# Optimization experiments

Hardware: AMD Instinct MI355X
Metric: run time of the kernel (lower is better)

The kernel has to match this reference:

```python
import jax, jax.numpy as jnp
import numpy as np

B, T, I, H, O, P = 32, 8192, 16, 128, 3, 1024


def setup_inputs() -> dict:
    key = jax.random.key(0)
    ks = jax.random.split(key, 8)
    x = jax.random.normal(ks[0], (B, T, I), dtype=jnp.float32)
    # feature channel 2 holds the photo id (original code does x[:,:,2].long())
    ids = jax.random.randint(ks[1], (B, T), 0, P)
    x = x.at[:, :, 2].set(ids.astype(jnp.float32))
    s = 1.0 / np.sqrt(H).astype(np.float32)
    W_ih = jax.random.uniform(ks[2], (4 * H, I), minval=-s, maxval=s, dtype=jnp.float32)
    W_hh = jax.random.uniform(ks[3], (4 * H, H), minval=-s, maxval=s, dtype=jnp.float32)
    b_ih = jax.random.uniform(ks[4], (4 * H,), minval=-s, maxval=s, dtype=jnp.float32)
    b_hh = jax.random.uniform(ks[5], (4 * H,), minval=-s, maxval=s, dtype=jnp.float32)
    W_fc = jax.random.uniform(ks[6], (O, H), minval=-s, maxval=s, dtype=jnp.float32)
    b_fc = jax.random.uniform(ks[7], (O,), minval=-s, maxval=s, dtype=jnp.float32)
    return dict(x=x, W_ih=W_ih, W_hh=W_hh, b_ih=b_ih, b_hh=b_hh,
                W_fc=W_fc, b_fc=b_fc, num_photos=P)


def _lstm(x, W_ih, W_hh, b_ih, b_hh):
    # single-layer batch_first LSTM, PyTorch gate order (i, f, g, o), zero init state
    Bz = x.shape[0]
    Hh = W_hh.shape[1]
    # precompute input contribution for all timesteps: [B, T, 4H]
    xg = jnp.einsum('bti,gi->btg', x, W_ih) + b_ih + b_hh

    def step(carry, gx):
        h, c = carry
        g = gx + h @ W_hh.T
        i, f, gg, o = jnp.split(g, 4, axis=-1)
        i = jax.nn.sigmoid(i)
        f = jax.nn.sigmoid(f)
        gg = jnp.tanh(gg)
        o = jax.nn.sigmoid(o)
        c = f * c + i * gg
        h = o * jnp.tanh(c)
        return (h, c), h

    h0 = jnp.zeros((Bz, Hh), x.dtype)
    _, hs = jax.lax.scan(step, (h0, h0), jnp.swapaxes(xg, 0, 1))  # [T, B, H]
    return jnp.swapaxes(hs, 0, 1)  # [B, T, H]


def reference(x, W_ih, W_hh, b_ih, b_hh, W_fc, b_fc, num_photos):
    Bz, T, _ = x.shape
    h = _lstm(x, W_ih, W_hh, b_ih, b_hh)          # [B, T, H]
    out = h @ W_fc.T + b_fc                        # [B, T, 3]
    ids = x[:, :, 2].astype(jnp.int32)             # [B, T]
    valid = ids < num_photos
    safe = jnp.where(valid, ids, 0)
    # flatten (batch, photo_id) into a single segment id per element
    seg = (jnp.arange(Bz, dtype=jnp.int32)[:, None] * num_photos + safe).reshape(-1)
    w = valid.astype(out.dtype)
    sums = jax.ops.segment_sum((out * w[..., None]).reshape(-1, out.shape[-1]),
                               seg, num_segments=Bz * num_photos)
    sums = sums.reshape(Bz, num_photos, out.shape[-1])
    counts = jax.ops.segment_sum(w.reshape(-1), seg, num_segments=Bz * num_photos)
    counts = counts.reshape(Bz, num_photos, 1)
    counts = jnp.where(counts == 0, 1.0, counts)   # matches photo_counts[photo_counts==0]=1
    return sums / counts
```

## Files before the change

### kernel.cpp

```cpp
#include <hip/hip_runtime.h>

#define B_ 32
#define T_ 8192
#define I_ 16
#define H_ 128
#define P_ 1024
#define O_ 3

typedef _Float16 h2 __attribute__((ext_vector_type(2)));
typedef _Float16 h4 __attribute__((ext_vector_type(4)));
typedef _Float16 h8 __attribute__((ext_vector_type(8)));

#if __has_builtin(__builtin_amdgcn_fdot2)
#define FDOT2(a, b, c) __builtin_amdgcn_fdot2((a), (b), (c), false)
#else
__device__ __forceinline__ float fdot2_asm(h2 a, h2 b, float c) {
    asm("v_dot2_f32_f16 %0, %1, %2, %0" : "+v"(c) : "v"(a), "v"(b));
    return c;
}
#define FDOT2(a, b, c) fdot2_asm((a), (b), (c))
#endif

#define FORME(M, g) M(g,0,0) M(g,0,1) M(g,0,2) M(g,0,3) \
                    M(g,1,0) M(g,1,1) M(g,1,2) M(g,1,3) \
                    M(g,2,0) M(g,2,1) M(g,2,2) M(g,2,3) \
                    M(g,3,0) M(g,3,1) M(g,3,2) M(g,3,3)
#define FORALL(M) FORME(M,0) FORME(M,1) FORME(M,2) FORME(M,3)
#define FORG(M) M(0) M(1) M(2) M(3)

#define DPPF(v, ctrl) \
    __int_as_float(__builtin_amdgcn_mov_dpp(__float_as_int(v), (ctrl), 0xF, 0xF, true))
#define SWZF(v, imm) \
    __int_as_float(__builtin_amdgcn_ds_swizzle(__float_as_int(v), (imm)))

__device__ __forceinline__ float tanh_f(float x) {
    return 2.f / (1.f + __expf(-2.f * x)) - 1.f;
}
__device__ __forceinline__ h4 cvt4(float4 v) {
    return (h4){(_Float16)v.x, (_Float16)v.y, (_Float16)v.z, (_Float16)v.w};
}

__device__ __forceinline__ void lds_barrier() {
    asm volatile("s_waitcnt lgkmcnt(0)\n\ts_barrier" ::: "memory");
}

__global__ __launch_bounds__(512, 2) __attribute__((amdgpu_waves_per_eu(2, 2)))
void lstm_fused(
    const float* __restrict__ x,
    const float* __restrict__ W_ih,
    const float* __restrict__ W_hh,
    const float* __restrict__ b_ih,
    const float* __restrict__ b_hh,
    const float* __restrict__ W_fc,
    float* __restrict__ sums,
    float* __restrict__ counts)
{
    const int b   = blockIdx.x;
    const int tid = threadIdx.x;
    const int j   = tid >> 2;
    const int kc  = tid & 3;

    __shared__ __align__(16) _Float16 hh[2][H_];
    __shared__ __align__(16) _Float16 xt[2][16 * I_];
    __shared__ float sums_lds[P_ * O_];
    __shared__ float counts_lds[P_];

    const float* wr0 = W_hh + (0 * H_ + j) * H_;
    const float* wr1 = W_hh + (1 * H_ + j) * H_;
    const float* wr2 = W_hh + (2 * H_ + j) * H_;
    const float* wr3 = W_hh + (3 * H_ + j) * H_;
    #define WLOAD(g, m, e) h2 W##g##_##m##_##e = (h2){ \
        (_Float16)wr##g[kc * 8 + 32 * (m) + 2 * (e)], \
        (_Float16)wr##g[kc * 8 + 32 * (m) + 2 * (e) + 1]};
    FORALL(WLOAD)

    #define ULOAD(g) \
        h2 U##g##_0 = (h2){(_Float16)W_ih[((g) * H_ + j) * I_ + kc * 4 + 0], \
                           (_Float16)W_ih[((g) * H_ + j) * I_ + kc * 4 + 1]}; \
        h2 U##g##_1 = (h2){(_Float16)W_ih[((g) * H_ + j) * I_ + kc * 4 + 2], \
                           (_Float16)W_ih[((g) * H_ + j) * I_ + kc * 4 + 3]};
    FORG(ULOAD)

    const float bias = b_ih[kc * H_ + j] + b_hh[kc * H_ + j];
    const float wfc  = (kc < 3) ? W_fc[kc * H_ + j] : 0.f;

    for (int i = tid; i < P_ * O_; i += 512) sums_lds[i] = 0.f;
    for (int i = tid; i < P_;      i += 512) counts_lds[i] = 0.f;
    if (tid < H_) hh[0][tid] = (_Float16)0.f;

    const float* xb = x + (size_t)b * T_ * I_;
    float4 xr4 = make_float4(0.f, 0.f, 0.f, 0.f);
    if (tid < 64) {
        xr4 = ((const float4*)xb)[tid];
        *(h4*)&xt[0][tid * 4] = cvt4(xr4);
    }
    float c = 0.f;
    __syncthreads();

    #pragma unroll 1
    for (int t = 0; t < T_; ++t) {
        const int off = t & 15;
        const int btx = (t >> 4) & 1;
        const int bh  = t & 1;

        if (tid < 64) {
            if (off == 0 && t + 16 < T_)
                xr4 = ((const float4*)(xb + (t + 16) * I_))[tid];
            if (off == 8 && t + 8 < T_)
                *(h4*)&xt[btx ^ 1][tid * 4] = cvt4(xr4);
        }

        const h4 xv4 = *(const h4*)&xt[btx][off * I_ + kc * 4];
        const h2 xv0 = __builtin_shufflevector(xv4, xv4, 0, 1);
        const h2 xv1 = __builtin_shufflevector(xv4, xv4, 2, 3);
        const int id = (int)(float)xt[btx][off * I_ + 2];

        float acc0 = 0.f, acc1 = 0.f, acc2 = 0.f, acc3 = 0.f;
        #define HD(m) { \
            h8 hv = *(const h8*)&hh[bh][kc * 8 + 32 * (m)]; \
            h2 p0 = __builtin_shufflevector(hv, hv, 0, 1); \
            h2 p1 = __builtin_shufflevector(hv, hv, 2, 3); \
            h2 p2 = __builtin_shufflevector(hv, hv, 4, 5); \
            h2 p3 = __builtin_shufflevector(hv, hv, 6, 7); \
            acc0 = FDOT2(p0, W0_##m##_0, acc0); acc0 = FDOT2(p1, W0_##m##_1, acc0); \
            acc0 = FDOT2(p2, W0_##m##_2, acc0); acc0 = FDOT2(p3, W0_##m##_3, acc0); \
            acc1 = FDOT2(p0, W1_##m##_0, acc1); acc1 = FDOT2(p1, W1_##m##_1, acc1); \
            acc1 = FDOT2(p2, W1_##m##_2, acc1); acc1 = FDOT2(p3, W1_##m##_3, acc1); \
            acc2 = FDOT2(p0, W2_##m##_0, acc2); acc2 = FDOT2(p1, W2_##m##_1, acc2); \
            acc2 = FDOT2(p2, W2_##m##_2, acc2); acc2 = FDOT2(p3, W2_##m##_3, acc2); \
            acc3 = FDOT2(p0, W3_##m##_0, acc3); acc3 = FDOT2(p1, W3_##m##_1, acc3); \
            acc3 = FDOT2(p2, W3_##m##_2, acc3); acc3 = FDOT2(p3, W3_##m##_3, acc3); }
        HD(0) HD(1) HD(2) HD(3)
        acc0 = FDOT2(xv0, U0_0, acc0); acc0 = FDOT2(xv1, U0_1, acc0);
        acc1 = FDOT2(xv0, U1_0, acc1); acc1 = FDOT2(xv1, U1_1, acc1);
        acc2 = FDOT2(xv0, U2_0, acc2); acc2 = FDOT2(xv1, U2_1, acc2);
        acc3 = FDOT2(xv0, U3_0, acc3); acc3 = FDOT2(xv1, U3_1, acc3);

        float s_;
        s_ = DPPF(acc0, 0xB1); acc0 += s_;
        s_ = DPPF(acc1, 0xB1); acc1 += s_;
        s_ = DPPF(acc2, 0xB1); acc2 += s_;
        s_ = DPPF(acc3, 0xB1); acc3 += s_;
        s_ = DPPF(acc0, 0x4E); acc0 += s_;
        s_ = DPPF(acc1, 0x4E); acc1 += s_;
        s_ = DPPF(acc2, 0x4E); acc2 += s_;
        s_ = DPPF(acc3, 0x4E); acc3 += s_;

        float tg = (kc == 0) ? acc0 : (kc == 1) ? acc1 : (kc == 2) ? acc2 : acc3;
        tg += bias;
        const bool  isg = (kc == 2);
        const float arg = isg ? (tg + tg) : tg;
        const float sf  = 1.f / (1.f + __expf(-arg));
        const float act = isg ? (sf + sf - 1.f) : sf;

        const float gi = DPPF(act, 0x00);
        const float gf = DPPF(act, 0x55);
        const float gg = DPPF(act, 0xAA);
        const float go = DPPF(act, 0xFF);
        c = fmaf(gf, c, gi * gg);
        const float hnew = go * tanh_f(c);

        if (kc == 0) hh[bh ^ 1][j] = (_Float16)hnew;

        float p = hnew * wfc;
        p += SWZF(p, 0x101F);
        p += SWZF(p, 0x201F);
        p += SWZF(p, 0x401F);
        p += __shfl_xor(p, 32, 64);
        const bool idv = ((unsigned)id < P_);
        if (((tid & 63) < 3) && idv)
            atomicAdd(&sums_lds[id * O_ + (tid & 63)], p);
        if (tid == 0 && idv)
            atomicAdd(&counts_lds[id], 1.f);

        lds_barrier();
    }

    float* sums_g = sums + (size_t)b * P_ * O_;
    for (int i = tid; i < P_ * O_; i += 512) sums_g[i] = sums_lds[i];
    float* cnt_g = counts + (size_t)b * P_;
    for (int i = tid; i < P_; i += 512) cnt_g[i] = counts_lds[i];
}

__global__ void finalize_kernel(const float* __restrict__ sums,
                                const float* __restrict__ counts,
                                const float* __restrict__ b_fc,
                                float* __restrict__ out)
{
    const int idx = blockIdx.x * blockDim.x + threadIdx.x;
    if (idx >= B_ * P_ * O_) return;
    const int o  = idx % O_;
    const int bp = idx / O_;
    const float cnt = counts[bp];
    const float denom = (cnt > 0.f) ? cnt : 1.f;
    out[idx] = (sums[idx] + cnt * b_fc[o]) / denom;
}

extern "C" void kernel_launch(void* const* d_in, const int* in_sizes, int n_in,
                              void* d_out, int out_size, void* d_ws, size_t ws_size,
                              hipStream_t stream) {
    const float* x    = (const float*)d_in[0];
    const float* W_ih = (const float*)d_in[1];
    const float* W_hh = (const float*)d_in[2];
    const float* b_ih = (const float*)d_in[3];
    const float* b_hh = (const float*)d_in[4];
    const float* W_fc = (const float*)d_in[5];
    const float* b_fc = (const float*)d_in[6];

    float* out    = (float*)d_out;
    float* sums   = (float*)d_ws;
    float* counts = sums + (size_t)B_ * P_ * O_;

    lstm_fused<<<B_, 512, 0, stream>>>(x, W_ih, W_hh, b_ih, b_hh, W_fc, sums, counts);

    const int n = B_ * P_ * O_;
    finalize_kernel<<<(n + 255) / 256, 256, 0, stream>>>(sums, counts, b_fc, out);
}
```

Before: 6.346 ms.

## Batch four sequences per block and compute LSTM recurrence with MFMA

Replaces the per-sequence fdot2 recurrence with 16x16x32 f16 MFMA instructions, processing four batch sequences per block (8 blocks instead of 32), with N columns replicated across the four sequences. Gate preactivations, bias, and the input projection are folded into MFMA accumulation, and the hidden state is stored in a skewed LDS layout to avoid bank conflicts. Segment atomics are deferred one step to overlap with the next step's compute. This trades parallelism across CUs for matrix-core throughput, so the serial per-step latency now decides the speed.

```diff
diff --git a/kernel.cpp b/kernel.cpp
--- a/kernel.cpp
+++ b/kernel.cpp
@@ -6,45 +6,35 @@
 #define H_ 128
 #define P_ 1024
 #define O_ 3
-
-typedef _Float16 h2 __attribute__((ext_vector_type(2)));
-typedef _Float16 h4 __attribute__((ext_vector_type(4)));
-typedef _Float16 h8 __attribute__((ext_vector_type(8)));
-
-#if __has_builtin(__builtin_amdgcn_fdot2)
-#define FDOT2(a, b, c) __builtin_amdgcn_fdot2((a), (b), (c), false)
-#else
-__device__ __forceinline__ float fdot2_asm(h2 a, h2 b, float c) {
-    asm("v_dot2_f32_f16 %0, %1, %2, %0" : "+v"(c) : "v"(a), "v"(b));
-    return c;
-}
-#define FDOT2(a, b, c) fdot2_asm((a), (b), (c))
-#endif
-
-#define FORME(M, g) M(g,0,0) M(g,0,1) M(g,0,2) M(g,0,3) \
-                    M(g,1,0) M(g,1,1) M(g,1,2) M(g,1,3) \
-                    M(g,2,0) M(g,2,1) M(g,2,2) M(g,2,3) \
-                    M(g,3,0) M(g,3,1) M(g,3,2) M(g,3,3)
-#define FORALL(M) FORME(M,0) FORME(M,1) FORME(M,2) FORME(M,3)
-#define FORG(M) M(0) M(1) M(2) M(3)
-
-#define DPPF(v, ctrl) \
-    __int_as_float(__builtin_amdgcn_mov_dpp(__float_as_int(v), (ctrl), 0xF, 0xF, true))
+#define NB 4
+#define BLOCKS (B_ / NB)
+
+typedef _Float16 h4v __attribute__((ext_vector_type(4)));
+typedef _Float16 h8v __attribute__((ext_vector_type(8)));
+typedef float f4v __attribute__((ext_vector_type(4)));
+
 #define SWZF(v, imm) \
     __int_as_float(__builtin_amdgcn_ds_swizzle(__float_as_int(v), (imm)))
-
+__device__ __forceinline__ float xor32_add(float p) {
+    float a = p, b = p;
+    asm("v_permlane32_swap_b32 %0, %1" : "+v"(a), "+v"(b));
+    return a + b;
+}
+
+__device__ __forceinline__ float sigf(float x) {
+    return 1.f / (1.f + __expf(-x));
+}
 __device__ __forceinline__ float tanh_f(float x) {
     return 2.f / (1.f + __expf(-2.f * x)) - 1.f;
 }
-__device__ __forceinline__ h4 cvt4(float4 v) {
-    return (h4){(_Float16)v.x, (_Float16)v.y, (_Float16)v.z, (_Float16)v.w};
-}
-
+__device__ __forceinline__ h4v cvt4(float4 v) {
+    return (h4v){(_Float16)v.x, (_Float16)v.y, (_Float16)v.z, (_Float16)v.w};
+}
 __device__ __forceinline__ void lds_barrier() {
     asm volatile("s_waitcnt lgkmcnt(0)\n\ts_barrier" ::: "memory");
 }
 
-__global__ __launch_bounds__(512, 2) __attribute__((amdgpu_waves_per_eu(2, 2)))
+__global__ __launch_bounds__(512, 2)
 void lstm_fused(
     const float* __restrict__ x,
     const float* __restrict__ W_ih,
@@ -55,131 +45,175 @@
     float* __restrict__ sums,
     float* __restrict__ counts)
 {
-    const int b   = blockIdx.x;
-    const int tid = threadIdx.x;
-    const int j   = tid >> 2;
-    const int kc  = tid & 3;
-
-    __shared__ __align__(16) _Float16 hh[2][H_];
-    __shared__ __align__(16) _Float16 xt[2][16 * I_];
-    __shared__ float sums_lds[P_ * O_];
-    __shared__ float counts_lds[P_];
-
-    const float* wr0 = W_hh + (0 * H_ + j) * H_;
-    const float* wr1 = W_hh + (1 * H_ + j) * H_;
-    const float* wr2 = W_hh + (2 * H_ + j) * H_;
-    const float* wr3 = W_hh + (3 * H_ + j) * H_;
-    #define WLOAD(g, m, e) h2 W##g##_##m##_##e = (h2){ \
-        (_Float16)wr##g[kc * 8 + 32 * (m) + 2 * (e)], \
-        (_Float16)wr##g[kc * 8 + 32 * (m) + 2 * (e) + 1]};
-    FORALL(WLOAD)
-
-    #define ULOAD(g) \
-        h2 U##g##_0 = (h2){(_Float16)W_ih[((g) * H_ + j) * I_ + kc * 4 + 0], \
-                           (_Float16)W_ih[((g) * H_ + j) * I_ + kc * 4 + 1]}; \
-        h2 U##g##_1 = (h2){(_Float16)W_ih[((g) * H_ + j) * I_ + kc * 4 + 2], \
-                           (_Float16)W_ih[((g) * H_ + j) * I_ + kc * 4 + 3]};
-    FORG(ULOAD)
-
-    const float bias = b_ih[kc * H_ + j] + b_hh[kc * H_ + j];
-    const float wfc  = (kc < 3) ? W_fc[kc * H_ + j] : 0.f;
-
-    for (int i = tid; i < P_ * O_; i += 512) sums_lds[i] = 0.f;
-    for (int i = tid; i < P_;      i += 512) counts_lds[i] = 0.f;
-    if (tid < H_) hh[0][tid] = (_Float16)0.f;
-
-    const float* xb = x + (size_t)b * T_ * I_;
+    const int bx   = blockIdx.x;
+    const int tid  = threadIdx.x;
+    const int w    = tid >> 6;
+    const int lane = tid & 63;
+    const int n    = lane & 15;
+    const int gh   = lane >> 4;
+    const int j0   = 16 * w + 4 * gh;
+
+    __shared__ float sums_lds[NB][P_ * O_];
+    __shared__ float counts_lds[NB][P_];
+    __shared__ __align__(16) _Float16 Hlds[2][16][H_];
+    __shared__ __align__(16) _Float16 xt[2][16][NB][I_];
+
+    h8v A[4][5];
+    #pragma unroll
+    for (int G = 0; G < 4; ++G) {
+        const int row = 128 * G + 16 * w + n;
+        const float* wr = W_hh + (size_t)row * H_;
+        #pragma unroll
+        for (int kt = 0; kt < 4; ++kt) {
+            h8v f;
+            #pragma unroll
+            for (int i = 0; i < 8; ++i)
+                f[i] = (_Float16)wr[32 * kt + 8 * gh + i];
+            A[G][kt] = f;
+        }
+        h8v fx = (h8v){(_Float16)0.f, (_Float16)0.f, (_Float16)0.f, (_Float16)0.f,
+                       (_Float16)0.f, (_Float16)0.f, (_Float16)0.f, (_Float16)0.f};
+        if (gh < 2) {
+            #pragma unroll
+            for (int i = 0; i < 8; ++i)
+                fx[i] = (_Float16)W_ih[(size_t)row * I_ + 8 * gh + i];
+        }
+        A[G][4] = fx;
+    }
+
+    f4v biasv[4];
+    #pragma unroll
+    for (int G = 0; G < 4; ++G) {
+        f4v bv;
+        #pragma unroll
+        for (int r = 0; r < 4; ++r)
+            bv[r] = b_ih[128 * G + j0 + r] + b_hh[128 * G + j0 + r];
+        biasv[G] = bv;
+    }
+
+    float wfc0[4], wfc1[4], wfc2[4];
+    #pragma unroll
+    for (int r = 0; r < 4; ++r) {
+        wfc0[r] = W_fc[0 * H_ + j0 + r];
+        wfc1[r] = W_fc[1 * H_ + j0 + r];
+        wfc2[r] = W_fc[2 * H_ + j0 + r];
+    }
+
+    for (int i = tid; i < NB * P_ * O_; i += 512) ((float*)sums_lds)[i] = 0.f;
+    for (int i = tid; i < NB * P_;      i += 512) ((float*)counts_lds)[i] = 0.f;
+    for (int i = tid; i < 2 * 16 * H_;  i += 512) ((_Float16*)Hlds)[i] = (_Float16)0.f;
+
+    const int pb = (tid >> 6) & 3;
+    const int r6 = tid & 63;
+    const int ps = r6 >> 2;
+    const int pe = r6 & 3;
+    const float* xb_pb = x + (size_t)(NB * bx + pb) * T_ * I_;
     float4 xr4 = make_float4(0.f, 0.f, 0.f, 0.f);
-    if (tid < 64) {
-        xr4 = ((const float4*)xb)[tid];
-        *(h4*)&xt[0][tid * 4] = cvt4(xr4);
-    }
-    float c = 0.f;
+    if (tid < 256) {
+        xr4 = *(const float4*)&xb_pb[ps * I_ + pe * 4];
+        *(h4v*)&xt[0][ps][pb][pe * 4] = cvt4(xr4);
+    }
+
+    float cc[4] = {0.f, 0.f, 0.f, 0.f};
+    float pp0 = 0.f, pp1 = 0.f, pp2 = 0.f;
+    int pid = P_;
     __syncthreads();
 
     #pragma unroll 1
     for (int t = 0; t < T_; ++t) {
         const int off = t & 15;
         const int btx = (t >> 4) & 1;
-        const int bh  = t & 1;
-
-        if (tid < 64) {
+        const int par = t & 1;
+
+        if (t != 0 && lane < NB && (unsigned)pid < (unsigned)P_) {
+            atomicAdd(&sums_lds[lane][pid * O_ + 0], pp0);
+            atomicAdd(&sums_lds[lane][pid * O_ + 1], pp1);
+            atomicAdd(&sums_lds[lane][pid * O_ + 2], pp2);
+            if (w == 0) atomicAdd(&counts_lds[lane][pid], 1.f);
+        }
+
+        if (tid < 256) {
             if (off == 0 && t + 16 < T_)
-                xr4 = ((const float4*)(xb + (t + 16) * I_))[tid];
+                xr4 = *(const float4*)&xb_pb[(t + 16 + ps) * I_ + pe * 4];
             if (off == 8 && t + 8 < T_)
-                *(h4*)&xt[btx ^ 1][tid * 4] = cvt4(xr4);
-        }
-
-        const h4 xv4 = *(const h4*)&xt[btx][off * I_ + kc * 4];
-        const h2 xv0 = __builtin_shufflevector(xv4, xv4, 0, 1);
-        const h2 xv1 = __builtin_shufflevector(xv4, xv4, 2, 3);
-        const int id = (int)(float)xt[btx][off * I_ + 2];
-
-        float acc0 = 0.f, acc1 = 0.f, acc2 = 0.f, acc3 = 0.f;
-        #define HD(m) { \
-            h8 hv = *(const h8*)&hh[bh][kc * 8 + 32 * (m)]; \
-            h2 p0 = __builtin_shufflevector(hv, hv, 0, 1); \
-            h2 p1 = __builtin_shufflevector(hv, hv, 2, 3); \
-            h2 p2 = __builtin_shufflevector(hv, hv, 4, 5); \
-            h2 p3 = __builtin_shufflevector(hv, hv, 6, 7); \
-            acc0 = FDOT2(p0, W0_##m##_0, acc0); acc0 = FDOT2(p1, W0_##m##_1, acc0); \
-            acc0 = FDOT2(p2, W0_##m##_2, acc0); acc0 = FDOT2(p3, W0_##m##_3, acc0); \
-            acc1 = FDOT2(p0, W1_##m##_0, acc1); acc1 = FDOT2(p1, W1_##m##_1, acc1); \
-            acc1 = FDOT2(p2, W1_##m##_2, acc1); acc1 = FDOT2(p3, W1_##m##_3, acc1); \
-            acc2 = FDOT2(p0, W2_##m##_0, acc2); acc2 = FDOT2(p1, W2_##m##_1, acc2); \
-            acc2 = FDOT2(p2, W2_##m##_2, acc2); acc2 = FDOT2(p3, W2_##m##_3, acc2); \
-            acc3 = FDOT2(p0, W3_##m##_0, acc3); acc3 = FDOT2(p1, W3_##m##_1, acc3); \
-            acc3 = FDOT2(p2, W3_##m##_2, acc3); acc3 = FDOT2(p3, W3_##m##_3, acc3); }
-        HD(0) HD(1) HD(2) HD(3)
-        acc0 = FDOT2(xv0, U0_0, acc0); acc0 = FDOT2(xv1, U0_1, acc0);
-        acc1 = FDOT2(xv0, U1_0, acc1); acc1 = FDOT2(xv1, U1_1, acc1);
-        acc2 = FDOT2(xv0, U2_0, acc2); acc2 = FDOT2(xv1, U2_1, acc2);
-        acc3 = FDOT2(xv0, U3_0, acc3); acc3 = FDOT2(xv1, U3_1, acc3);
-
-        float s_;
-        s_ = DPPF(acc0, 0xB1); acc0 += s_;
-        s_ = DPPF(acc1, 0xB1); acc1 += s_;
-        s_ = DPPF(acc2, 0xB1); acc2 += s_;
-        s_ = DPPF(acc3, 0xB1); acc3 += s_;
-        s_ = DPPF(acc0, 0x4E); acc0 += s_;
-        s_ = DPPF(acc1, 0x4E); acc1 += s_;
-        s_ = DPPF(acc2, 0x4E); acc2 += s_;
-        s_ = DPPF(acc3, 0x4E); acc3 += s_;
-
-        float tg = (kc == 0) ? acc0 : (kc == 1) ? acc1 : (kc == 2) ? acc2 : acc3;
-        tg += bias;
-        const bool  isg = (kc == 2);
-        const float arg = isg ? (tg + tg) : tg;
-        const float sf  = 1.f / (1.f + __expf(-arg));
-        const float act = isg ? (sf + sf - 1.f) : sf;
-
-        const float gi = DPPF(act, 0x00);
-        const float gf = DPPF(act, 0x55);
-        const float gg = DPPF(act, 0xAA);
-        const float go = DPPF(act, 0xFF);
-        c = fmaf(gf, c, gi * gg);
-        const float hnew = go * tanh_f(c);
-
-        if (kc == 0) hh[bh ^ 1][j] = (_Float16)hnew;
-
-        float p = hnew * wfc;
-        p += SWZF(p, 0x101F);
-        p += SWZF(p, 0x201F);
-        p += SWZF(p, 0x401F);
-        p += __shfl_xor(p, 32, 64);
-        const bool idv = ((unsigned)id < P_);
-        if (((tid & 63) < 3) && idv)
-            atomicAdd(&sums_lds[id * O_ + (tid & 63)], p);
-        if (tid == 0 && idv)
-            atomicAdd(&counts_lds[id], 1.f);
+                *(h4v*)&xt[btx ^ 1][ps][pb][pe * 4] = cvt4(xr4);
+        }
+
+        h8v Bf0 = *(const h8v*)&Hlds[par][n][(  0 + 8 * gh + 8 * n) & 127];
+        h8v Bf1 = *(const h8v*)&Hlds[par][n][( 32 + 8 * gh + 8 * n) & 127];
+        h8v Bf2 = *(const h8v*)&Hlds[par][n][( 64 + 8 * gh + 8 * n) & 127];
+        h8v Bf3 = *(const h8v*)&Hlds[par][n][( 96 + 8 * gh + 8 * n) & 127];
+        h8v bxf = (h8v){(_Float16)0.f, (_Float16)0.f, (_Float16)0.f, (_Float16)0.f,
+                        (_Float16)0.f, (_Float16)0.f, (_Float16)0.f, (_Float16)0.f};
+        if (gh < 2)
+            bxf = *(const h8v*)&xt[btx][off][n & 3][gh * 8];
+        const int idn = (int)(float)xt[btx][off][n & 3][2];
+
+        f4v acc[4];
+        #pragma unroll
+        for (int G = 0; G < 4; ++G)
+            acc[G] = __builtin_amdgcn_mfma_f32_16x16x32_f16(A[G][0], Bf0, biasv[G], 0, 0, 0);
+        #pragma unroll
+        for (int G = 0; G < 4; ++G)
+            acc[G] = __builtin_amdgcn_mfma_f32_16x16x32_f16(A[G][1], Bf1, acc[G], 0, 0, 0);
+        #pragma unroll
+        for (int G = 0; G < 4; ++G)
+            acc[G] = __builtin_amdgcn_mfma_f32_16x16x32_f16(A[G][2], Bf2, acc[G], 0, 0, 0);
+        #pragma unroll
+        for (int G = 0; G < 4; ++G)
+            acc[G] = __builtin_amdgcn_mfma_f32_16x16x32_f16(A[G][3], Bf3, acc[G], 0, 0, 0);
+        #pragma unroll
+        for (int G = 0; G < 4; ++G)
+            acc[G] = __builtin_amdgcn_mfma_f32_16x16x32_f16(A[G][4], bxf, acc[G], 0, 0, 0);
+
+        float hv[4];
+        #pragma unroll
+        for (int r = 0; r < 4; ++r) {
+            const float gi = sigf(acc[0][r]);
+            const float gf = sigf(acc[1][r]);
+            const float gg = tanh_f(acc[2][r]);
+            const float go = sigf(acc[3][r]);
+            cc[r] = fmaf(gf, cc[r], gi * gg);
+            hv[r] = go * tanh_f(cc[r]);
+        }
+
+        h4v hp = (h4v){(_Float16)hv[0], (_Float16)hv[1],
+                       (_Float16)hv[2], (_Float16)hv[3]};
+        *(h4v*)&Hlds[par ^ 1][n][(j0 + 8 * n) & 127] = hp;
+
+        float p0 = 0.f, p1 = 0.f, p2 = 0.f;
+        #pragma unroll
+        for (int r = 0; r < 4; ++r) {
+            p0 = fmaf(wfc0[r], hv[r], p0);
+            p1 = fmaf(wfc1[r], hv[r], p1);
+            p2 = fmaf(wfc2[r], hv[r], p2);
+        }
+        p0 += SWZF(p0, 0x401F);
+        p1 += SWZF(p1, 0x401F);
+        p2 += SWZF(p2, 0x401F);
+        p0 = xor32_add(p0);
+        p1 = xor32_add(p1);
+        p2 = xor32_add(p2);
+        pp0 = p0; pp1 = p1; pp2 = p2;
+        pid = idn;
 
         lds_barrier();
     }
 
-    float* sums_g = sums + (size_t)b * P_ * O_;
-    for (int i = tid; i < P_ * O_; i += 512) sums_g[i] = sums_lds[i];
-    float* cnt_g = counts + (size_t)b * P_;
-    for (int i = tid; i < P_; i += 512) cnt_g[i] = counts_lds[i];
+    if (lane < NB && (unsigned)pid < (unsigned)P_) {
+        atomicAdd(&sums_lds[lane][pid * O_ + 0], pp0);
+        atomicAdd(&sums_lds[lane][pid * O_ + 1], pp1);
+        atomicAdd(&sums_lds[lane][pid * O_ + 2], pp2);
+        if (w == 0) atomicAdd(&counts_lds[lane][pid], 1.f);
+    }
+    __syncthreads();
+
+    float* sums_g = sums + (size_t)(NB * bx) * P_ * O_;
+    for (int i = tid; i < NB * P_ * O_; i += 512)
+        sums_g[i] = ((const float*)sums_lds)[i];
+    float* cnt_g = counts + (size_t)(NB * bx) * P_;
+    for (int i = tid; i < NB * P_; i += 512)
+        cnt_g[i] = ((const float*)counts_lds)[i];
 }
 
 __global__ void finalize_kernel(const float* __restrict__ sums,
@@ -211,7 +245,8 @@
     float* sums   = (float*)d_ws;
     float* counts = sums + (size_t)B_ * P_ * O_;
 
-    lstm_fused<<<B_, 512, 0, stream>>>(x, W_ih, W_hh, b_ih, b_hh, W_fc, sums, counts);
+    lstm_fused<<<BLOCKS, 512, 0, stream>>>(x, W_ih, W_hh, b_ih, b_hh, W_fc,
+                                           sums, counts);
 
     const int n = B_ * P_ * O_;
     finalize_kernel<<<(n + 255) / 256, 256, 0, stream>>>(sums, counts, b_fc, out);
```

Result: slower. 14.18 ms (+123.5%).
